# Kernel optimization log

Hardware: AMD Instinct MI355X
Metric: run time of the kernel (lower is better)

The kernel has to match this reference:

```python
import jax, jax.numpy as jnp
import numpy as np

T, H, I, E, K = 4096, 2048, 4096, 8, 2

def setup_inputs() -> dict:
    key = jax.random.key(0)
    k1, k2, k3, k4, k5 = jax.random.split(key, 5)
    return {
        "hidden_states": jax.random.normal(k1, (T, H), dtype=jnp.float32),
        "topk_weights": jax.random.uniform(k2, (T, K), dtype=jnp.float32, minval=0.01, maxval=1.0),
        "topk_ids": jax.random.randint(k3, (T, K), 0, E, dtype=jnp.int64),
        "gate_up_weights": jax.random.normal(k4, (E, 2 * I, H), dtype=jnp.float32) * 0.02,
        "down_weights": jax.random.normal(k5, (E, H, I), dtype=jnp.float32) * 0.02,
    }

def reference(hidden_states, topk_weights, topk_ids, gate_up_weights, down_weights):
    # renormalize=True: per-token top-k weights sum to 1
    tw = topk_weights / jnp.sum(topk_weights, axis=-1, keepdims=True)  # [T, K]
    n_experts = gate_up_weights.shape[0]
    # per-expert combine weight for each token: sum of tw where routed to expert e -> [E, T]
    expert_w = jax.vmap(
        lambda e: jnp.sum(jnp.where(topk_ids == e, tw, 0.0), axis=-1)
    )(jnp.arange(n_experts))

    def body(acc, ew):
        gu, dw, w = ew  # gu: [2I, H], dw: [H, I], w: [T]
        h = hidden_states @ gu.T            # [T, 2I]
        gate, up = jnp.split(h, 2, axis=-1)  # silu_and_mul epilogue
        act = jax.nn.silu(gate) * up        # [T, I]
        out_e = act @ dw.T                  # [T, H]
        return acc + w[:, None] * out_e, None

    init = jnp.zeros_like(hidden_states)
    out, _ = jax.lax.scan(body, init, (gate_up_weights, down_weights, expert_w))
    return out
```

## Files before the change

### kernel.cpp

```cpp
#include <hip/hip_runtime.h>


#define T_TOK 4096
#define H_DIM 2048
#define I_DIM 4096
#define E_NUM 8
#define K_TOP 2
#define NSLOT (T_TOK * K_TOP)

#define BM 128
#define BN 128
#define BK 64
#define LDKO 72

typedef float f32x4 __attribute__((ext_vector_type(4)));
typedef __bf16 bf16x8 __attribute__((ext_vector_type(8)));
typedef unsigned int u32x4 __attribute__((ext_vector_type(4)));

static __device__ __forceinline__ unsigned short f2bf(float f) {
  unsigned u = __float_as_uint(f);
  u += 0x7FFFu + ((u >> 16) & 1u);
  return (unsigned short)(u >> 16);
}

static __device__ __forceinline__ unsigned long long pack4bf(float x0, float x1, float x2, float x3) {
  unsigned lo = (unsigned)f2bf(x0) | ((unsigned)f2bf(x1) << 16);
  unsigned hi = (unsigned)f2bf(x2) | ((unsigned)f2bf(x3) << 16);
  return (unsigned long long)lo | ((unsigned long long)hi << 32);
}

static __device__ __forceinline__ void gload16(void* lds, const void* g) {
  __builtin_amdgcn_global_load_lds(
      (const __attribute__((address_space(1))) unsigned int*)(g),
      (__attribute__((address_space(3))) unsigned int*)(lds), 16, 0, 0);
}

__global__ void routing_kernel(const float* __restrict__ tw,
                               const int* __restrict__ ids,
                               int* __restrict__ offsets,
                               int* __restrict__ stok,
                               float* __restrict__ sw,
                               int* __restrict__ slot_of) {
  __shared__ int cnt[E_NUM];
  __shared__ int cur[E_NUM];
  __shared__ int basesh[E_NUM + 1];
  int tid = threadIdx.x;
  if (tid < E_NUM) cnt[tid] = 0;
  __syncthreads();
  for (int idx = tid; idx < NSLOT; idx += 256) atomicAdd(&cnt[ids[idx]], 1);
  __syncthreads();
  if (tid == 0) {
    int acc = 0;
    for (int e = 0; e < E_NUM; ++e) { basesh[e] = acc; acc += cnt[e]; }
    basesh[E_NUM] = acc;
    for (int e = 0; e <= E_NUM; ++e) offsets[e] = basesh[e];
  }
  __syncthreads();
  if (tid < E_NUM) cur[tid] = basesh[tid];
  __syncthreads();
  for (int idx = tid; idx < NSLOT; idx += 256) {
    int t = idx >> 1;
    float w0 = tw[t * 2], w1 = tw[t * 2 + 1];
    float w = ((idx & 1) ? w1 : w0) / (w0 + w1);
    int e = ids[idx];
    int slot = atomicAdd(&cur[e], 1);
    stok[slot] = t;
    sw[slot] = w;
    slot_of[idx] = slot;
  }
}

__global__ __launch_bounds__(256) void cvt_bf16_kernel(const float* __restrict__ in,
                                                       unsigned short* __restrict__ out,
                                                       long long n8) {
  long long stride = (long long)gridDim.x * 256;
  for (long long i = (long long)blockIdx.x * 256 + threadIdx.x; i < n8; i += stride) {
    long long o = i * 8;
    f32x4 v0 = *(const f32x4*)(in + o);
    f32x4 v1 = *(const f32x4*)(in + o + 4);
    unsigned long long p0 = pack4bf(v0[0], v0[1], v0[2], v0[3]);
    unsigned long long p1 = pack4bf(v1[0], v1[1], v1[2], v1[3]);
    u32x4 st;
    st[0] = (unsigned)p0; st[1] = (unsigned)(p0 >> 32);
    st[2] = (unsigned)p1; st[3] = (unsigned)(p1 >> 32);
    *(u32x4*)(out + o) = st;
  }
}

__global__ __launch_bounds__(256, 2) void gemm1_bf16_kernel(
    const unsigned short* __restrict__ hb,
    const unsigned short* __restrict__ gub,
    const int* __restrict__ offsets, const int* __restrict__ stok,
    unsigned short* __restrict__ act) {
  int e = blockIdx.z;
  int base = offsets[e];
  int cnt = offsets[e + 1] - base;
  int m0 = blockIdx.y * BM;
  if (m0 >= cnt) return;
  int n0 = blockIdx.x * BN;
  int rem = cnt - m0;

  __shared__ __attribute__((aligned(16))) unsigned short As[2][BM * 64];
  __shared__ __attribute__((aligned(16))) unsigned short Bg[BN * 64];
  __shared__ __attribute__((aligned(16))) unsigned short Bu[BN * 64];
  __shared__ int toks[BM];

  int tid = threadIdx.x;
  if (tid < BM) toks[tid] = (tid < rem) ? stok[base + m0 + tid] : stok[base];
  __syncthreads();

  int lane = tid & 63;
  int wid = tid >> 6;
  int srow = lane >> 3;
  int scol = ((lane & 7) ^ srow) << 3;

  const unsigned short* wrow = gub + (size_t)e * (2 * (size_t)I_DIM) * H_DIM;
  const unsigned short* pa[4];
  const unsigned short* pg[4];
  const unsigned short* pu[4];
#pragma unroll
  for (int s = 0; s < 4; ++s) {
    int row = wid * 32 + s * 8 + srow;
    pa[s] = hb + (size_t)toks[row] * H_DIM + scol;
    pg[s] = wrow + (size_t)(n0 + row) * H_DIM + scol;
    pu[s] = wrow + (size_t)(I_DIM + n0 + row) * H_DIM + scol;
  }

  int lm = lane & 15;
  int q = lane >> 4;
  int wm = (wid >> 1) * 64;
  int wn = (wid & 1) * 64;
  int rc0 = ((q ^ (lm & 7)) << 3);
  int rc1 = (((4 + q) ^ (lm & 7)) << 3);

  f32x4 accg[4][4] = {};
  f32x4 accu[4][4] = {};

#pragma unroll
  for (int s = 0; s < 4; ++s)
    gload16(&As[0][(wid * 32 + s * 8) * 64], pa[s]);

  int cur = 0;
  for (int kb = 0; kb < H_DIM; kb += BK) {
#pragma unroll
    for (int s = 0; s < 4; ++s) {
      gload16(&Bg[(wid * 32 + s * 8) * 64], pg[s] + kb);
      gload16(&Bu[(wid * 32 + s * 8) * 64], pu[s] + kb);
    }
    if (kb + BK < H_DIM) {
#pragma unroll
      for (int s = 0; s < 4; ++s)
        gload16(&As[cur ^ 1][(wid * 32 + s * 8) * 64], pa[s] + kb + BK);
      __builtin_amdgcn_sched_barrier(0);
      asm volatile("s_waitcnt vmcnt(4)" ::: "memory");
    } else {
      __builtin_amdgcn_sched_barrier(0);
      asm volatile("s_waitcnt vmcnt(0)" ::: "memory");
    }
    __builtin_amdgcn_s_barrier();
    __builtin_amdgcn_sched_barrier(0);
#pragma unroll
    for (int ks = 0; ks < 2; ++ks) {
      int ko = ks ? rc1 : rc0;
      bf16x8 a[4], bg[4], bu[4];
#pragma unroll
      for (int i = 0; i < 4; ++i)
        a[i] = *(const bf16x8*)&As[cur][(wm + i * 16 + lm) * 64 + ko];
#pragma unroll
      for (int j = 0; j < 4; ++j) {
        bg[j] = *(const bf16x8*)&Bg[(wn + j * 16 + lm) * 64 + ko];
        bu[j] = *(const bf16x8*)&Bu[(wn + j * 16 + lm) * 64 + ko];
      }
#pragma unroll
      for (int i = 0; i < 4; ++i)
#pragma unroll
        for (int j = 0; j < 4; ++j) {
          accg[i][j] = __builtin_amdgcn_mfma_f32_16x16x32_bf16(a[i], bg[j], accg[i][j], 0, 0, 0);
          accu[i][j] = __builtin_amdgcn_mfma_f32_16x16x32_bf16(a[i], bu[j], accu[i][j], 0, 0, 0);
        }
    }
    __builtin_amdgcn_sched_barrier(0);
    __builtin_amdgcn_s_barrier();
    cur ^= 1;
  }

#pragma unroll
  for (int i = 0; i < 4; ++i) {
    int mb = wm + i * 16 + q * 4;
#pragma unroll
    for (int r = 0; r < 4; ++r) {
      int m = mb + r;
      if (m < rem) {
        size_t rowoff = (size_t)(base + m0 + m) * I_DIM + n0;
#pragma unroll
        for (int j = 0; j < 4; ++j) {
          int n = wn + j * 16 + lm;
          float g = accg[i][j][r];
          float u = accu[i][j][r];
          float aa = (g / (1.0f + __expf(-g))) * u;
          act[rowoff + n] = f2bf(aa);
        }
      }
    }
  }
}

__global__ __launch_bounds__(256, 3) void gemm2_bf16_kernel(
    const unsigned short* __restrict__ act, const unsigned short* __restrict__ dwb,
    const int* __restrict__ offsets, const float* __restrict__ sw,
    float* __restrict__ dout) {
  int e = blockIdx.z;
  int base = offsets[e];
  int cnt = offsets[e + 1] - base;
  int m0 = blockIdx.y * BM;
  if (m0 >= cnt) return;
  int n0 = blockIdx.x * BN;
  int rem = cnt - m0;

  __shared__ __attribute__((aligned(16))) unsigned short As[2][BM * 64];
  __shared__ __attribute__((aligned(16))) unsigned short Bs[BN * 64];
  __shared__ float wsl[BM];

  int tid = threadIdx.x;
  if (tid < BM) wsl[tid] = (tid < rem) ? sw[base + m0 + tid] : 0.f;
  __syncthreads();

  int lane = tid & 63;
  int wid = tid >> 6;
  int srow = lane >> 3;
  int scol = ((lane & 7) ^ srow) << 3;

  const unsigned short* dp = dwb + (size_t)e * ((size_t)H_DIM * I_DIM);
  const unsigned short* pa[4];
  const unsigned short* pb[4];
#pragma unroll
  for (int s = 0; s < 4; ++s) {
    int row = wid * 32 + s * 8 + srow;
    pa[s] = act + (size_t)(base + m0 + row) * I_DIM + scol;
    pb[s] = dp + (size_t)(n0 + row) * I_DIM + scol;
  }

  int lm = lane & 15;
  int q = lane >> 4;
  int wm = (wid >> 1) * 64;
  int wn = (wid & 1) * 64;
  int rc0 = ((q ^ (lm & 7)) << 3);
  int rc1 = (((4 + q) ^ (lm & 7)) << 3);

  f32x4 acc[4][4] = {};

#pragma unroll
  for (int s = 0; s < 4; ++s)
    gload16(&As[0][(wid * 32 + s * 8) * 64], pa[s]);

  int cur = 0;
  for (int kb = 0; kb < I_DIM; kb += BK) {
#pragma unroll
    for (int s = 0; s < 4; ++s)
      gload16(&Bs[(wid * 32 + s * 8) * 64], pb[s] + kb);
    if (kb + BK < I_DIM) {
#pragma unroll
      for (int s = 0; s < 4; ++s)
        gload16(&As[cur ^ 1][(wid * 32 + s * 8) * 64], pa[s] + kb + BK);
      __builtin_amdgcn_sched_barrier(0);
      asm volatile("s_waitcnt vmcnt(4)" ::: "memory");
    } else {
      __builtin_amdgcn_sched_barrier(0);
      asm volatile("s_waitcnt vmcnt(0)" ::: "memory");
    }
    __builtin_amdgcn_s_barrier();
    __builtin_amdgcn_sched_barrier(0);
#pragma unroll
    for (int ks = 0; ks < 2; ++ks) {
      int ko = ks ? rc1 : rc0;
      bf16x8 a[4], b[4];
#pragma unroll
      for (int i = 0; i < 4; ++i)
        a[i] = *(const bf16x8*)&As[cur][(wm + i * 16 + lm) * 64 + ko];
#pragma unroll
      for (int j = 0; j < 4; ++j)
        b[j] = *(const bf16x8*)&Bs[(wn + j * 16 + lm) * 64 + ko];
#pragma unroll
      for (int i = 0; i < 4; ++i)
#pragma unroll
        for (int j = 0; j < 4; ++j)
          acc[i][j] = __builtin_amdgcn_mfma_f32_16x16x32_bf16(a[i], b[j], acc[i][j], 0, 0, 0);
    }
    __builtin_amdgcn_sched_barrier(0);
    __builtin_amdgcn_s_barrier();
    cur ^= 1;
  }

#pragma unroll
  for (int i = 0; i < 4; ++i) {
    int mb = wm + i * 16 + q * 4;
#pragma unroll
    for (int r = 0; r < 4; ++r) {
      int m = mb + r;
      if (m < rem) {
        float w = wsl[m];
        size_t rowoff = (size_t)(base + m0 + m) * H_DIM + n0;
#pragma unroll
        for (int j = 0; j < 4; ++j)
          dout[rowoff + wn + j * 16 + lm] = acc[i][j][r] * w;
      }
    }
  }
}

__global__ __launch_bounds__(256, 2) void gemm1_kernel(
    const float* __restrict__ hidden, const float* __restrict__ gu,
    const int* __restrict__ offsets, const int* __restrict__ stok,
    unsigned short* __restrict__ act) {
  int e = blockIdx.z;
  int base = offsets[e];
  int cnt = offsets[e + 1] - base;
  int m0 = blockIdx.y * BM;
  if (m0 >= cnt) return;
  int n0 = blockIdx.x * BN;
  int rem = cnt - m0;

  __shared__ unsigned short As[BM * LDKO];
  __shared__ unsigned short Bg[BM * LDKO];
  __shared__ unsigned short Bu[BM * LDKO];
  __shared__ int toks[BM];

  int tid = threadIdx.x;
  if (tid < BM) toks[tid] = (tid < rem) ? stok[base + m0 + tid] : -1;
  __syncthreads();

  int lane = tid & 63;
  int wid = tid >> 6;
  int wm = (wid >> 1) * 64;
  int wn = (wid & 1) * 64;
  int lm = lane & 15;
  int q = lane >> 4;

  f32x4 accg[4][4] = {};
  f32x4 accu[4][4] = {};
  const float* gup = gu + (size_t)e * (2 * (size_t)I_DIM * H_DIM);

  for (int kb = 0; kb < H_DIM; kb += 64) {
#pragma unroll
    for (int s = 0; s < 8; ++s) {
      int task = tid + s * 256;
      int row = task >> 4;
      int cg = (task & 15) << 2;
      int tok = toks[row];
      float x0 = 0.f, x1 = 0.f, x2 = 0.f, x3 = 0.f;
      if (tok >= 0) {
        f32x4 v = *(const f32x4*)(hidden + (size_t)tok * H_DIM + kb + cg);
        x0 = v[0]; x1 = v[1]; x2 = v[2]; x3 = v[3];
      }
      *(unsigned long long*)&As[row * LDKO + cg] = pack4bf(x0, x1, x2, x3);
    }
#pragma unroll
    for (int s = 0; s < 8; ++s) {
      int task = tid + s * 256;
      int row = task >> 4;
      int cg = (task & 15) << 2;
      f32x4 vg = *(const f32x4*)(gup + (size_t)(n0 + row) * H_DIM + kb + cg);
      f32x4 vu = *(const f32x4*)(gup + (size_t)(I_DIM + n0 + row) * H_DIM + kb + cg);
      *(unsigned long long*)&Bg[row * LDKO + cg] = pack4bf(vg[0], vg[1], vg[2], vg[3]);
      *(unsigned long long*)&Bu[row * LDKO + cg] = pack4bf(vu[0], vu[1], vu[2], vu[3]);
    }
    __syncthreads();
#pragma unroll
    for (int ks = 0; ks < 2; ++ks) {
      int ko = ks * 32 + q * 8;
      bf16x8 a[4], bg[4], bu[4];
#pragma unroll
      for (int i = 0; i < 4; ++i)
        a[i] = *(const bf16x8*)&As[(wm + i * 16 + lm) * LDKO + ko];
#pragma unroll
      for (int j = 0; j < 4; ++j) {
        bg[j] = *(const bf16x8*)&Bg[(wn + j * 16 + lm) * LDKO + ko];
        bu[j] = *(const bf16x8*)&Bu[(wn + j * 16 + lm) * LDKO + ko];
      }
#pragma unroll
      for (int i = 0; i < 4; ++i)
#pragma unroll
        for (int j = 0; j < 4; ++j) {
          accg[i][j] = __builtin_amdgcn_mfma_f32_16x16x32_bf16(a[i], bg[j], accg[i][j], 0, 0, 0);
          accu[i][j] = __builtin_amdgcn_mfma_f32_16x16x32_bf16(a[i], bu[j], accu[i][j], 0, 0, 0);
        }
    }
    __syncthreads();
  }

#pragma unroll
  for (int i = 0; i < 4; ++i) {
    int mb = wm + i * 16 + q * 4;
#pragma unroll
    for (int r = 0; r < 4; ++r) {
      int m = mb + r;
      if (m < rem) {
        size_t rowoff = (size_t)(base + m0 + m) * I_DIM + n0;
#pragma unroll
        for (int j = 0; j < 4; ++j) {
          int n = wn + j * 16 + lm;
          float g = accg[i][j][r];
          float u = accu[i][j][r];
          float aa = (g / (1.0f + __expf(-g))) * u;
          act[rowoff + n] = f2bf(aa);
        }
      }
    }
  }
}

__global__ __launch_bounds__(256, 2) void gemm2_kernel(
    const unsigned short* __restrict__ act, const float* __restrict__ dwn,
    const int* __restrict__ offsets, const float* __restrict__ sw,
    float* __restrict__ dout) {
  int e = blockIdx.z;
  int base = offsets[e];
  int cnt = offsets[e + 1] - base;
  int m0 = blockIdx.y * BM;
  if (m0 >= cnt) return;
  int n0 = blockIdx.x * BN;
  int rem = cnt - m0;

  __shared__ unsigned short As[BM * LDKO];
  __shared__ unsigned short Bs[BM * LDKO];
  __shared__ float wsl[BM];

  int tid = threadIdx.x;
  if (tid < BM) wsl[tid] = (tid < rem) ? sw[base + m0 + tid] : 0.f;

  int lane = tid & 63;
  int wid = tid >> 6;
  int wm = (wid >> 1) * 64;
  int wn = (wid & 1) * 64;
  int lm = lane & 15;
  int q = lane >> 4;

  f32x4 acc[4][4] = {};
  const float* dp = dwn + (size_t)e * ((size_t)H_DIM * I_DIM);
  const unsigned short* ap = act + (size_t)(base + m0) * I_DIM;

  for (int kb = 0; kb < I_DIM; kb += 64) {
#pragma unroll
    for (int s = 0; s < 4; ++s) {
      int task = tid + s * 256;
      int row = task >> 3;
      int cg = (task & 7) << 3;
      u32x4 v = *(const u32x4*)(ap + (size_t)row * I_DIM + kb + cg);
      *(u32x4*)&As[row * LDKO + cg] = v;
    }
#pragma unroll
    for (int s = 0; s < 8; ++s) {
      int task = tid + s * 256;
      int row = task >> 4;
      int cg = (task & 15) << 2;
      f32x4 v = *(const f32x4*)(dp + (size_t)(n0 + row) * I_DIM + kb + cg);
      *(unsigned long long*)&Bs[row * LDKO + cg] = pack4bf(v[0], v[1], v[2], v[3]);
    }
    __syncthreads();
#pragma unroll
    for (int ks = 0; ks < 2; ++ks) {
      int ko = ks * 32 + q * 8;
      bf16x8 a[4], b[4];
#pragma unroll
      for (int i = 0; i < 4; ++i)
        a[i] = *(const bf16x8*)&As[(wm + i * 16 + lm) * LDKO + ko];
#pragma unroll
      for (int j = 0; j < 4; ++j)
        b[j] = *(const bf16x8*)&Bs[(wn + j * 16 + lm) * LDKO + ko];
#pragma unroll
      for (int i = 0; i < 4; ++i)
#pragma unroll
        for (int j = 0; j < 4; ++j)
          acc[i][j] = __builtin_amdgcn_mfma_f32_16x16x32_bf16(a[i], b[j], acc[i][j], 0, 0, 0);
    }
    __syncthreads();
  }

#pragma unroll
  for (int i = 0; i < 4; ++i) {
    int mb = wm + i * 16 + q * 4;
#pragma unroll
    for (int r = 0; r < 4; ++r) {
      int m = mb + r;
      if (m < rem) {
        float w = wsl[m];
        size_t rowoff = (size_t)(base + m0 + m) * H_DIM + n0;
#pragma unroll
        for (int j = 0; j < 4; ++j)
          dout[rowoff + wn + j * 16 + lm] = acc[i][j][r] * w;
      }
    }
  }
}

__global__ void combine_kernel(const f32x4* __restrict__ dout4,
                               const int* __restrict__ slot_of,
                               f32x4* __restrict__ out4) {
  int idx = blockIdx.x * 256 + threadIdx.x;
  int t = idx >> 9;
  int c = idx & 511;
  int s0 = slot_of[t * 2];
  int s1 = slot_of[t * 2 + 1];
  f32x4 r = dout4[(size_t)s0 * 512 + c] + dout4[(size_t)s1 * 512 + c];
  out4[idx] = r;
}

extern "C" void kernel_launch(void* const* d_in, const int* in_sizes, int n_in,
                              void* d_out, int out_size, void* d_ws, size_t ws_size,
                              hipStream_t stream) {
  const float* hidden = (const float*)d_in[0];
  const float* tw     = (const float*)d_in[1];
  const int*   ids    = (const int*)d_in[2];
  const float* gu     = (const float*)d_in[3];
  const float* dwn    = (const float*)d_in[4];
  float* out = (float*)d_out;
  char* ws = (char*)d_ws;

  int*   offsets = (int*)ws;
  int*   stok    = (int*)(ws + 256);
  float* swp     = (float*)(ws + 256 + 32768);
  int*   slot_of = (int*)(ws + 256 + 65536);
  const size_t base_off = 1 << 17;
  const size_t act_sz   = (size_t)(NSLOT + BM) * I_DIM * 2;

  routing_kernel<<<1, 256, 0, stream>>>(tw, ids, offsets, stok, swp, slot_of);

  const size_t hb_sz  = (size_t)T_TOK * H_DIM * 2;
  const size_t gu_sz  = (size_t)E_NUM * 2 * (size_t)I_DIM * H_DIM * 2;
  const size_t dwn_sz = (size_t)E_NUM * (size_t)H_DIM * I_DIM * 2;
  const size_t w_off  = base_off + hb_sz;
  const size_t need   = w_off + gu_sz + act_sz;

  if (ws_size >= need) {
    unsigned short* hb   = (unsigned short*)(ws + base_off);
    unsigned short* gub  = (unsigned short*)(ws + w_off);
    unsigned short* dwb  = (unsigned short*)(ws + w_off);
    float*          dout = (float*)(ws + w_off + dwn_sz);
    unsigned short* act  = (unsigned short*)(ws + w_off + gu_sz);

    cvt_bf16_kernel<<<2048, 256, 0, stream>>>(hidden, hb, (long long)T_TOK * H_DIM / 8);
    cvt_bf16_kernel<<<2048, 256, 0, stream>>>(gu, gub, (long long)E_NUM * 2 * I_DIM * H_DIM / 8);
    gemm1_bf16_kernel<<<dim3(I_DIM / BN, NSLOT / BM, E_NUM), 256, 0, stream>>>(hb, gub, offsets, stok, act);
    cvt_bf16_kernel<<<2048, 256, 0, stream>>>(dwn, dwb, (long long)E_NUM * H_DIM * I_DIM / 8);
    gemm2_bf16_kernel<<<dim3(H_DIM / BN, NSLOT / BM, E_NUM), 256, 0, stream>>>(act, dwb, offsets, swp, dout);
    combine_kernel<<<(T_TOK * H_DIM / 4) / 256, 256, 0, stream>>>((const f32x4*)dout, slot_of, (f32x4*)out);
  } else {
    unsigned short* act  = (unsigned short*)(ws + base_off);
    float*          dout = (float*)(ws + base_off + act_sz);
    gemm1_kernel<<<dim3(I_DIM / BN, NSLOT / BM, E_NUM), 256, 0, stream>>>(hidden, gu, offsets, stok, act);
    gemm2_kernel<<<dim3(H_DIM / BN, NSLOT / BM, E_NUM), 256, 0, stream>>>(act, dwn, offsets, swp, dout);
    combine_kernel<<<(T_TOK * H_DIM / 4) / 256, 256, 0, stream>>>((const f32x4*)dout, slot_of, (f32x4*)out);
  }
}
```

Baseline: 1.452 ms.

## Use 512-thread blocks and double-buffer weight tiles in bf16 MoE GEMMs

Both bf16 GEMM kernels move from 4 to 8 waves per block, with each wave computing a 64x32 sub-tile instead of 64x64. The B tiles (gate/up or down weights) become double-buffered so they are prefetched one K step ahead together with the A tile, instead of being loaded at the start of each iteration. The aim is to hide global load latency for the weights and raise wave-level parallelism. LDS use per block grows and launch bounds change, which may reduce resident blocks per CU.

Result: slower. 1.662 ms (+14.5%).

```diff
diff --git a/kernel.cpp b/kernel.cpp
--- a/kernel.cpp
+++ b/kernel.cpp
@@ -87,7 +87,7 @@
   }
 }
 
-__global__ __launch_bounds__(256, 2) void gemm1_bf16_kernel(
+__global__ __launch_bounds__(512, 2) void gemm1_bf16_kernel(
     const unsigned short* __restrict__ hb,
     const unsigned short* __restrict__ gub,
     const int* __restrict__ offsets, const int* __restrict__ stok,
@@ -101,8 +101,8 @@
   int rem = cnt - m0;
 
   __shared__ __attribute__((aligned(16))) unsigned short As[2][BM * 64];
-  __shared__ __attribute__((aligned(16))) unsigned short Bg[BN * 64];
-  __shared__ __attribute__((aligned(16))) unsigned short Bu[BN * 64];
+  __shared__ __attribute__((aligned(16))) unsigned short Bg[2][BM * 64];
+  __shared__ __attribute__((aligned(16))) unsigned short Bu[2][BM * 64];
   __shared__ int toks[BM];
 
   int tid = threadIdx.x;
@@ -111,48 +111,50 @@
 
   int lane = tid & 63;
   int wid = tid >> 6;
-  int srow = lane >> 3;
-  int scol = ((lane & 7) ^ srow) << 3;
+  int r0 = tid >> 3;
+  int scol = ((tid & 7) ^ (r0 & 7)) << 3;
 
   const unsigned short* wrow = gub + (size_t)e * (2 * (size_t)I_DIM) * H_DIM;
-  const unsigned short* pa[4];
-  const unsigned short* pg[4];
-  const unsigned short* pu[4];
-#pragma unroll
-  for (int s = 0; s < 4; ++s) {
-    int row = wid * 32 + s * 8 + srow;
+  const unsigned short* pa[2];
+  const unsigned short* pg[2];
+  const unsigned short* pu[2];
+#pragma unroll
+  for (int s = 0; s < 2; ++s) {
+    int row = s * 64 + r0;
     pa[s] = hb + (size_t)toks[row] * H_DIM + scol;
     pg[s] = wrow + (size_t)(n0 + row) * H_DIM + scol;
     pu[s] = wrow + (size_t)(I_DIM + n0 + row) * H_DIM + scol;
   }
+  int ldo = tid * 8;
 
   int lm = lane & 15;
   int q = lane >> 4;
-  int wm = (wid >> 1) * 64;
-  int wn = (wid & 1) * 64;
+  int wm = (wid >> 2) * 64;
+  int wn = (wid & 3) * 32;
   int rc0 = ((q ^ (lm & 7)) << 3);
   int rc1 = (((4 + q) ^ (lm & 7)) << 3);
 
-  f32x4 accg[4][4] = {};
-  f32x4 accu[4][4] = {};
-
-#pragma unroll
-  for (int s = 0; s < 4; ++s)
-    gload16(&As[0][(wid * 32 + s * 8) * 64], pa[s]);
+  f32x4 accg[4][2] = {};
+  f32x4 accu[4][2] = {};
+
+  auto stage = [&](int b, int kbo) {
+#pragma unroll
+    for (int s = 0; s < 2; ++s) {
+      int d = ldo + s * 4096;
+      gload16(&As[b][d], pa[s] + kbo);
+      gload16(&Bg[b][d], pg[s] + kbo);
+      gload16(&Bu[b][d], pu[s] + kbo);
+    }
+  };
+
+  stage(0, 0);
 
   int cur = 0;
   for (int kb = 0; kb < H_DIM; kb += BK) {
-#pragma unroll
-    for (int s = 0; s < 4; ++s) {
-      gload16(&Bg[(wid * 32 + s * 8) * 64], pg[s] + kb);
-      gload16(&Bu[(wid * 32 + s * 8) * 64], pu[s] + kb);
-    }
     if (kb + BK < H_DIM) {
-#pragma unroll
-      for (int s = 0; s < 4; ++s)
-        gload16(&As[cur ^ 1][(wid * 32 + s * 8) * 64], pa[s] + kb + BK);
+      stage(cur ^ 1, kb + BK);
       __builtin_amdgcn_sched_barrier(0);
-      asm volatile("s_waitcnt vmcnt(4)" ::: "memory");
+      asm volatile("s_waitcnt vmcnt(6)" ::: "memory");
     } else {
       __builtin_amdgcn_sched_barrier(0);
       asm volatile("s_waitcnt vmcnt(0)" ::: "memory");
@@ -162,19 +164,19 @@
 #pragma unroll
     for (int ks = 0; ks < 2; ++ks) {
       int ko = ks ? rc1 : rc0;
-      bf16x8 a[4], bg[4], bu[4];
+      bf16x8 a[4], bg[2], bu[2];
 #pragma unroll
       for (int i = 0; i < 4; ++i)
         a[i] = *(const bf16x8*)&As[cur][(wm + i * 16 + lm) * 64 + ko];
 #pragma unroll
-      for (int j = 0; j < 4; ++j) {
-        bg[j] = *(const bf16x8*)&Bg[(wn + j * 16 + lm) * 64 + ko];
-        bu[j] = *(const bf16x8*)&Bu[(wn + j * 16 + lm) * 64 + ko];
-      }
-#pragma unroll
-      for (int i = 0; i < 4; ++i)
-#pragma unroll
-        for (int j = 0; j < 4; ++j) {
+      for (int j = 0; j < 2; ++j) {
+        bg[j] = *(const bf16x8*)&Bg[cur][(wn + j * 16 + lm) * 64 + ko];
+        bu[j] = *(const bf16x8*)&Bu[cur][(wn + j * 16 + lm) * 64 + ko];
+      }
+#pragma unroll
+      for (int i = 0; i < 4; ++i)
+#pragma unroll
+        for (int j = 0; j < 2; ++j) {
           accg[i][j] = __builtin_amdgcn_mfma_f32_16x16x32_bf16(a[i], bg[j], accg[i][j], 0, 0, 0);
           accu[i][j] = __builtin_amdgcn_mfma_f32_16x16x32_bf16(a[i], bu[j], accu[i][j], 0, 0, 0);
         }
@@ -193,7 +195,7 @@
       if (m < rem) {
         size_t rowoff = (size_t)(base + m0 + m) * I_DIM + n0;
 #pragma unroll
-        for (int j = 0; j < 4; ++j) {
+        for (int j = 0; j < 2; ++j) {
           int n = wn + j * 16 + lm;
           float g = accg[i][j][r];
           float u = accu[i][j][r];
@@ -205,7 +207,7 @@
   }
 }
 
-__global__ __launch_bounds__(256, 3) void gemm2_bf16_kernel(
+__global__ __launch_bounds__(512, 4) void gemm2_bf16_kernel(
     const unsigned short* __restrict__ act, const unsigned short* __restrict__ dwb,
     const int* __restrict__ offsets, const float* __restrict__ sw,
     float* __restrict__ dout) {
@@ -218,7 +220,7 @@
   int rem = cnt - m0;
 
   __shared__ __attribute__((aligned(16))) unsigned short As[2][BM * 64];
-  __shared__ __attribute__((aligned(16))) unsigned short Bs[BN * 64];
+  __shared__ __attribute__((aligned(16))) unsigned short Bs[2][BM * 64];
   __shared__ float wsl[BM];
 
   int tid = threadIdx.x;
@@ -227,41 +229,44 @@
 
   int lane = tid & 63;
   int wid = tid >> 6;
-  int srow = lane >> 3;
-  int scol = ((lane & 7) ^ srow) << 3;
+  int r0 = tid >> 3;
+  int scol = ((tid & 7) ^ (r0 & 7)) << 3;
 
   const unsigned short* dp = dwb + (size_t)e * ((size_t)H_DIM * I_DIM);
-  const unsigned short* pa[4];
-  const unsigned short* pb[4];
-#pragma unroll
-  for (int s = 0; s < 4; ++s) {
-    int row = wid * 32 + s * 8 + srow;
+  const unsigned short* pa[2];
+  const unsigned short* pb[2];
+#pragma unroll
+  for (int s = 0; s < 2; ++s) {
+    int row = s * 64 + r0;
     pa[s] = act + (size_t)(base + m0 + row) * I_DIM + scol;
     pb[s] = dp + (size_t)(n0 + row) * I_DIM + scol;
   }
+  int ldo = tid * 8;
 
   int lm = lane & 15;
   int q = lane >> 4;
-  int wm = (wid >> 1) * 64;
-  int wn = (wid & 1) * 64;
+  int wm = (wid >> 2) * 64;
+  int wn = (wid & 3) * 32;
   int rc0 = ((q ^ (lm & 7)) << 3);
   int rc1 = (((4 + q) ^ (lm & 7)) << 3);
 
-  f32x4 acc[4][4] = {};
-
-#pragma unroll
-  for (int s = 0; s < 4; ++s)
-    gload16(&As[0][(wid * 32 + s * 8) * 64], pa[s]);
+  f32x4 acc[4][2] = {};
+
+  auto stage = [&](int b, int kbo) {
+#pragma unroll
+    for (int s = 0; s < 2; ++s) {
+      int d = ldo + s * 4096;
+      gload16(&As[b][d], pa[s] + kbo);
+      gload16(&Bs[b][d], pb[s] + kbo);
+    }
+  };
+
+  stage(0, 0);
 
   int cur = 0;
   for (int kb = 0; kb < I_DIM; kb += BK) {
-#pragma unroll
-    for (int s = 0; s < 4; ++s)
-      gload16(&Bs[(wid * 32 + s * 8) * 64], pb[s] + kb);
     if (kb + BK < I_DIM) {
-#pragma unroll
-      for (int s = 0; s < 4; ++s)
-        gload16(&As[cur ^ 1][(wid * 32 + s * 8) * 64], pa[s] + kb + BK);
+      stage(cur ^ 1, kb + BK);
       __builtin_amdgcn_sched_barrier(0);
       asm volatile("s_waitcnt vmcnt(4)" ::: "memory");
     } else {
@@ -273,17 +278,17 @@
 #pragma unroll
     for (int ks = 0; ks < 2; ++ks) {
       int ko = ks ? rc1 : rc0;
-      bf16x8 a[4], b[4];
+      bf16x8 a[4], b[2];
 #pragma unroll
       for (int i = 0; i < 4; ++i)
         a[i] = *(const bf16x8*)&As[cur][(wm + i * 16 + lm) * 64 + ko];
 #pragma unroll
-      for (int j = 0; j < 4; ++j)
-        b[j] = *(const bf16x8*)&Bs[(wn + j * 16 + lm) * 64 + ko];
-#pragma unroll
-      for (int i = 0; i < 4; ++i)
-#pragma unroll
-        for (int j = 0; j < 4; ++j)
+      for (int j = 0; j < 2; ++j)
+        b[j] = *(const bf16x8*)&Bs[cur][(wn + j * 16 + lm) * 64 + ko];
+#pragma unroll
+      for (int i = 0; i < 4; ++i)
+#pragma unroll
+        for (int j = 0; j < 2; ++j)
           acc[i][j] = __builtin_amdgcn_mfma_f32_16x16x32_bf16(a[i], b[j], acc[i][j], 0, 0, 0);
     }
     __builtin_amdgcn_sched_barrier(0);
@@ -301,7 +306,7 @@
         float w = wsl[m];
         size_t rowoff = (size_t)(base + m0 + m) * H_DIM + n0;
 #pragma unroll
-        for (int j = 0; j < 4; ++j)
+        for (int j = 0; j < 2; ++j)
           dout[rowoff + wn + j * 16 + lm] = acc[i][j][r] * w;
       }
     }
@@ -540,9 +545,9 @@
 
     cvt_bf16_kernel<<<2048, 256, 0, stream>>>(hidden, hb, (long long)T_TOK * H_DIM / 8);
     cvt_bf16_kernel<<<2048, 256, 0, stream>>>(gu, gub, (long long)E_NUM * 2 * I_DIM * H_DIM / 8);
-    gemm1_bf16_kernel<<<dim3(I_DIM / BN, NSLOT / BM, E_NUM), 256, 0, stream>>>(hb, gub, offsets, stok, act);
+    gemm1_bf16_kernel<<<dim3(I_DIM / BN, NSLOT / BM, E_NUM), 512, 0, stream>>>(hb, gub, offsets, stok, act);
     cvt_bf16_kernel<<<2048, 256, 0, stream>>>(dwn, dwb, (long long)E_NUM * H_DIM * I_DIM / 8);
-    gemm2_bf16_kernel<<<dim3(H_DIM / BN, NSLOT / BM, E_NUM), 256, 0, stream>>>(act, dwb, offsets, swp, dout);
+    gemm2_bf16_kernel<<<dim3(H_DIM / BN, NSLOT / BM, E_NUM), 512, 0, stream>>>(act, dwb, offsets, swp, dout);
     combine_kernel<<<(T_TOK * H_DIM / 4) / 256, 256, 0, stream>>>((const f32x4*)dout, slot_of, (f32x4*)out);
   } else {
     unsigned short* act  = (unsigned short*)(ws + base_off);
```
